# Performance work log

Hardware: AMD Instinct MI355X
Metric: run time of the kernel (lower is better)

Reference implementation:

```python
import jax, jax.numpy as jnp
import numpy as np

B, S, DM, H = 4, 1024, 1024, 16
D = DM // H  # attn_head_size = 64


def setup_inputs() -> dict:
    key = jax.random.key(0)
    ks = jax.random.split(key, 16)
    sc = 0.02
    return {
        "hidden_states": jax.random.normal(ks[0], (B, S, DM), jnp.float32),
        "wq": jax.random.normal(ks[1], (DM, DM), jnp.float32) * sc,
        "bq": jax.random.normal(ks[2], (DM,), jnp.float32) * sc,
        "wk": jax.random.normal(ks[3], (DM, DM), jnp.float32) * sc,
        "bk": jax.random.normal(ks[4], (DM,), jnp.float32) * sc,
        "wv": jax.random.normal(ks[5], (DM, DM), jnp.float32) * sc,
        "bv": jax.random.normal(ks[6], (DM,), jnp.float32) * sc,
        "wo": jax.random.normal(ks[7], (DM, DM), jnp.float32) * sc,
        "bo": jax.random.normal(ks[8], (DM,), jnp.float32) * sc,
        "wfq": jax.random.normal(ks[9], (DM, DM), jnp.float32) * sc,
        "bfq": jax.random.normal(ks[10], (DM,), jnp.float32) * sc,
        "wfg": jax.random.normal(ks[11], (DM, DM), jnp.float32) * sc,
        "bfg": jax.random.normal(ks[12], (DM,), jnp.float32) * sc,
        "up": jax.random.normal(ks[13], (H, 1, D), jnp.float32) * sc,
        "uz": jax.random.normal(ks[14], (H, 1, D), jnp.float32) * sc,
    }


def _split_heads(x):
    # [B, S, DM] -> [B, H, S, D]
    return x.reshape(x.shape[0], x.shape[1], H, D).transpose(0, 2, 1, 3)


def reference(hidden_states, wq, bq, wk, bk, wv, bv, wo, bo,
              wfq, bfq, wfg, bfg, up, uz):
    key_len = hidden_states.shape[1]
    mixed_q = hidden_states @ wq + bq  # [B, S, DM]
    mixed_k = hidden_states @ wk + bk
    mixed_v = hidden_states @ wv + bv

    # focus-attention Gaussian bias
    glo = jnp.mean(mixed_q, axis=1, keepdims=True)                      # [B, 1, DM]
    c = jnp.tanh((mixed_q @ wfq + bfq) + (glo @ wfg + bfg))             # [B, S, DM]
    c = _split_heads(c)                                                 # [B, H, S, D]
    p = jnp.sum(c * up[None], axis=-1)                                  # [B, H, S]
    z = jnp.sum(c * uz[None], axis=-1)                                  # [B, H, S]
    P = jax.nn.sigmoid(p) * key_len                                     # [B, H, S]
    Z = jax.nn.sigmoid(z) * key_len
    j = jnp.arange(key_len, dtype=P.dtype)                              # [S]
    # G[b,h,q,k] = -(k - P[b,h,q])^2 * 2 / Z[b,h,q]^2
    G = -((j[None, None, None, :] - P[..., None]) ** 2) * 2.0 / (Z[..., None] ** 2)

    q = _split_heads(mixed_q)
    k = _split_heads(mixed_k)
    v = _split_heads(mixed_v)

    scores = jnp.einsum("bhqd,bhkd->bhqk", q, k) / jnp.sqrt(jnp.float32(D))
    scores = scores + G
    probs = jax.nn.softmax(scores, axis=-1)  # dropout_prob = 0 -> no-op
    ctx = jnp.einsum("bhqk,bhkd->bhqd", probs, v)
    ctx = ctx.transpose(0, 2, 1, 3).reshape(ctx.shape[0], key_len, H * D)
    return ctx @ wo + bo
```

## Files before the change

kernel.cpp:

```cpp
#include <hip/hip_runtime.h>
#include <hip/hip_bf16.h>
#include <stdint.h>

#define DEV __device__ __forceinline__

typedef __attribute__((ext_vector_type(4))) float f32x4;
typedef __attribute__((ext_vector_type(8))) __bf16 bf16x8;
typedef __attribute__((ext_vector_type(4))) __bf16 bf16x4;
typedef __attribute__((ext_vector_type(4))) unsigned int uint4v;
typedef __attribute__((ext_vector_type(4))) int i32x4;

static constexpr int Bc = 4, Sc = 1024, DMc = 1024, Hc = 16, Dh = 64;
static constexpr int Mc = Bc * Sc;

DEV __bf16 f2b(float x) {
    unsigned u = __builtin_bit_cast(unsigned, x);
    unsigned r = (u + 0x7fffu + ((u >> 16) & 1u)) >> 16;
    return __builtin_bit_cast(__bf16, (unsigned short)r);
}
DEV float b2f(__bf16 x) {
    unsigned short s = __builtin_bit_cast(unsigned short, x);
    unsigned u = ((unsigned)s) << 16;
    return __builtin_bit_cast(float, u);
}
DEV unsigned cvt_pk_bf16(float a, float b) {
    unsigned r;
    asm("v_cvt_pk_bf16_f32 %0, %1, %2" : "=v"(r) : "v"(a), "v"(b));
    return r;
}
DEV void gload_lds16(const void* g, void* l) {
    __builtin_amdgcn_global_load_lds(
        (const __attribute__((address_space(1))) unsigned int*)g,
        (__attribute__((address_space(3))) unsigned int*)l,
        16, 0, 0);
}
DEV bf16x8 ldswz32(const __bf16* base, int row, int lg) {
    const char* p = (const char*)base + row * 64 + (((lg) ^ ((row >> 1) & 3)) << 4);
    return *(const bf16x8*)p;
}

__global__ void k_cvt2(const float* __restrict__ hs, __bf16* __restrict__ hsb,
                       float* __restrict__ part0) {
    int sc = blockIdx.x, b = blockIdx.y, tid = threadIdx.x;
    int c0 = tid * 4;
    float4 s = {0.f, 0.f, 0.f, 0.f};
#pragma unroll
    for (int r = 0; r < 8; r++) {
        size_t row = (size_t)b * 1024 + sc * 8 + r;
        float4 v = *(const float4*)&hs[row * 1024 + c0];
        s.x += v.x; s.y += v.y; s.z += v.z; s.w += v.w;
        bf16x4 o = { f2b(v.x), f2b(v.y), f2b(v.z), f2b(v.w) };
        *(bf16x4*)&hsb[row * 1024 + c0] = o;
    }
    *(float4*)&part0[(size_t)(sc * 4 + b) * 1024 + c0] = s;
}

__global__ void k_tcvt5(const float* __restrict__ s0, const float* __restrict__ s1,
                        const float* __restrict__ s2, const float* __restrict__ s3,
                        const float* __restrict__ s4,
                        __bf16* __restrict__ d0, __bf16* __restrict__ d1,
                        __bf16* __restrict__ d2, __bf16* __restrict__ d3,
                        __bf16* __restrict__ d4, __bf16* __restrict__ wqb) {
    __shared__ float t[32][33];
    const float* in; __bf16* out;
    switch (blockIdx.z) {
        case 0: in = s0; out = d0; break;
        case 1: in = s1; out = d1; break;
        case 2: in = s2; out = d2; break;
        case 3: in = s3; out = d3; break;
        default: in = s4; out = d4; break;
    }
    int c0 = blockIdx.x * 32, r0 = blockIdx.y * 32;
    for (int j = 0; j < 4; j++) {
        float v = in[(size_t)(r0 + threadIdx.y + j * 8) * 1024 + c0 + threadIdx.x];
        t[threadIdx.y + j * 8][threadIdx.x] = v;
        if (blockIdx.z == 0)
            wqb[(size_t)(r0 + threadIdx.y + j * 8) * 1024 + c0 + threadIdx.x] = f2b(v);
    }
    __syncthreads();
    for (int j = 0; j < 4; j++)
        out[(size_t)(c0 + threadIdx.y + j * 8) * 1024 + r0 + threadIdx.x] = f2b(t[threadIdx.x][threadIdx.y + j * 8]);
}

template <int EPI, int BM>
__global__ __launch_bounds__(256) void k_gemm(
    const __bf16* __restrict__ A, const __bf16* __restrict__ Bt,
    const float* __restrict__ bias, void* __restrict__ Cout, int N, int K)
{
    constexpr int MF = BM / 32;
    constexpr int ACH = BM / 64;
    __shared__ __bf16 Al[2][BM * 32];
    __shared__ __bf16 Bl[2][128 * 32];
    const int bm = blockIdx.x, bn = blockIdx.y;
    const int tid = threadIdx.x, lane = tid & 63, wid = tid >> 6;
    const int l15 = lane & 15, lg = lane >> 4;
    const int qr = (wid >> 1) * (BM / 2), qc = (wid & 1) * 64;
    f32x4 acc[MF][4] = {};

    const __bf16* Ab = A + (size_t)bm * BM * K;
    const __bf16* Bb = Bt + (size_t)bn * 128 * K;

#define STAGE_G(k0, dst)                                                          \
    _Pragma("unroll")                                                             \
    for (int c = 0; c < ACH; c++) {                                               \
        int ch = c * 256 + tid, row = ch >> 2, u = ch & 3;                        \
        int su = u ^ ((row >> 1) & 3);                                            \
        gload_lds16(&Ab[(size_t)row * K + (k0) + su * 8], &Al[dst][ch * 8]);      \
    }                                                                             \
    _Pragma("unroll")                                                             \
    for (int c = 0; c < 2; c++) {                                                 \
        int ch = c * 256 + tid, row = ch >> 2, u = ch & 3;                        \
        int su = u ^ ((row >> 1) & 3);                                            \
        gload_lds16(&Bb[(size_t)row * K + (k0) + su * 8], &Bl[dst][ch * 8]);      \
    }

    STAGE_G(0, 0);
    asm volatile("s_waitcnt vmcnt(0)" ::: "memory");
    __builtin_amdgcn_s_barrier();

    int buf = 0;
    for (int t = 0; t < K / 32; t++) {
        if (t + 1 < K / 32) { STAGE_G((t + 1) * 32, buf ^ 1); }
        bf16x8 af[MF], bfv[4];
#pragma unroll
        for (int m = 0; m < MF; m++) af[m] = ldswz32(&Al[buf][0], qr + m * 16 + l15, lg);
#pragma unroll
        for (int n = 0; n < 4; n++) bfv[n] = ldswz32(&Bl[buf][0], qc + n * 16 + l15, lg);
#pragma unroll
        for (int m = 0; m < MF; m++)
#pragma unroll
            for (int n = 0; n < 4; n++)
                acc[m][n] = __builtin_amdgcn_mfma_f32_16x16x32_bf16(af[m], bfv[n], acc[m][n], 0, 0, 0);
        asm volatile("s_waitcnt vmcnt(0)" ::: "memory");
        __builtin_amdgcn_s_barrier();
        buf ^= 1;
    }
#undef STAGE_G
#pragma unroll
    for (int m = 0; m < MF; m++) {
        int row_base = bm * BM + qr + m * 16 + lg * 4;
#pragma unroll
        for (int n = 0; n < 4; n++) {
            int col = bn * 128 + qc + n * 16 + l15;
            float bsum = bias ? bias[col] : 0.0f;
#pragma unroll
            for (int r = 0; r < 4; r++) {
                int row = row_base + r;
                float v = acc[m][n][r] + bsum;
                if constexpr (EPI == 2) ((float*)Cout)[(size_t)row * N + col] = v;
                else ((__bf16*)Cout)[(size_t)row * N + col] = f2b(v);
            }
        }
    }
}

__global__ __launch_bounds__(256) void k_qkvc(
    const __bf16* __restrict__ A, const __bf16* __restrict__ BtAll,
    const float* __restrict__ bq, const float* __restrict__ bk, const float* __restrict__ bv,
    const float* __restrict__ gt2, const float* __restrict__ up, const float* __restrict__ uz,
    __bf16* __restrict__ mq, __bf16* __restrict__ mk_, __bf16* __restrict__ vt,
    float* __restrict__ Pf, float* __restrict__ Zf)
{
    constexpr int K = 1024;
    __shared__ __bf16 Al[2][128 * 32];
    __shared__ __bf16 Bl[2][128 * 32];
    const int bm = blockIdx.x, bn = blockIdx.y;
    const int tid = threadIdx.x, lane = tid & 63, wid = tid >> 6;
    const int l15 = lane & 15, lg = lane >> 4;
    const int qr = (wid >> 1) * 64, qc = (wid & 1) * 64;
    f32x4 acc[4][4] = {};

    const __bf16* Ab = A + (size_t)bm * 128 * K;
    const __bf16* Bb = BtAll + (size_t)bn * 128 * K;

#define STAGE_Q(k0, dst)                                                          \
    _Pragma("unroll")                                                             \
    for (int c = 0; c < 2; c++) {                                                 \
        int ch = c * 256 + tid, row = ch >> 2, u = ch & 3;                        \
        int su = u ^ ((row >> 1) & 3);                                            \
        gload_lds16(&Ab[(size_t)row * K + (k0) + su * 8], &Al[dst][ch * 8]);      \
        gload_lds16(&Bb[(size_t)row * K + (k0) + su * 8], &Bl[dst][ch * 8]);      \
    }

    STAGE_Q(0, 0);
    asm volatile("s_waitcnt vmcnt(0)" ::: "memory");
    __builtin_amdgcn_s_barrier();

    int buf = 0;
    for (int t = 0; t < 32; t++) {
        if (t < 31) { STAGE_Q((t + 1) * 32, buf ^ 1); }
        bf16x8 af[4], bfv[4];
#pragma unroll
        for (int m = 0; m < 4; m++) af[m] = ldswz32(&Al[buf][0], qr + m * 16 + l15, lg);
#pragma unroll
        for (int n = 0; n < 4; n++) bfv[n] = ldswz32(&Bl[buf][0], qc + n * 16 + l15, lg);
#pragma unroll
        for (int m = 0; m < 4; m++)
#pragma unroll
            for (int n = 0; n < 4; n++)
                acc[m][n] = __builtin_amdgcn_mfma_f32_16x16x32_bf16(af[m], bfv[n], acc[m][n], 0, 0, 0);
        asm volatile("s_waitcnt vmcnt(0)" ::: "memory");
        __builtin_amdgcn_s_barrier();
        buf ^= 1;
    }
#undef STAGE_Q

    const int chunk = bn >> 3;
    if (chunk == 3) {
        const int h = (bn & 7) * 2 + (qc >> 6);
        float upv[4], uzv[4];
#pragma unroll
        for (int n = 0; n < 4; n++) {
            upv[n] = up[h * 64 + n * 16 + l15];
            uzv[n] = uz[h * 64 + n * 16 + l15];
        }
#pragma unroll
        for (int m = 0; m < 4; m++) {
            int row_base = bm * 128 + qr + m * 16 + lg * 4;
#pragma unroll
            for (int r = 0; r < 4; r++) {
                int row = row_base + r;
                float p = 0.f, z = 0.f;
#pragma unroll
                for (int n = 0; n < 4; n++) {
                    int col = (bn & 7) * 128 + qc + n * 16 + l15;
                    float cv = tanhf(acc[m][n][r] + gt2[(row >> 10) * 1024 + col]);
                    p += cv * upv[n];
                    z += cv * uzv[n];
                }
#pragma unroll
                for (int d = 1; d < 16; d <<= 1) {
                    p += __shfl_xor(p, d, 16);
                    z += __shfl_xor(z, d, 16);
                }
                if (l15 == 0) {
                    int bb = row >> 10, s = row & 1023;
                    Pf[((size_t)(bb * 16 + h)) * 1024 + s] = 1024.f / (1.f + __expf(-p));
                    Zf[((size_t)(bb * 16 + h)) * 1024 + s] = 1024.f / (1.f + __expf(-z));
                }
            }
        }
    } else if (chunk == 2) {
        const int b = bm >> 3;
#pragma unroll
        for (int m = 0; m < 4; m++) {
            int s0 = (bm & 7) * 128 + qr + m * 16 + lg * 4;
#pragma unroll
            for (int n = 0; n < 4; n++) {
                int col = (bn & 7) * 128 + qc + n * 16 + l15;
                int h = col >> 6, d = col & 63;
                float bsum = bv[col];
                bf16x4 o = { f2b(acc[m][n][0] + bsum), f2b(acc[m][n][1] + bsum),
                             f2b(acc[m][n][2] + bsum), f2b(acc[m][n][3] + bsum) };
                *(bf16x4*)&vt[((size_t)((b * 16 + h) * 64 + d)) * 1024 + s0] = o;
            }
        }
    } else {
        const float* bias = chunk == 0 ? bq : bk;
        __bf16* outp = chunk == 0 ? mq : mk_;
#pragma unroll
        for (int m = 0; m < 4; m++) {
            int row_base = bm * 128 + qr + m * 16 + lg * 4;
#pragma unroll
            for (int n = 0; n < 4; n++) {
                int col = (bn & 7) * 128 + qc + n * 16 + l15;
                float bsum = bias[col];
#pragma unroll
                for (int r = 0; r < 4; r++) {
                    int row = row_base + r;
                    outp[(size_t)row * 1024 + col] = f2b(acc[m][n][r] + bsum);
                }
            }
        }
    }
}

__global__ void k_glo2(const float* __restrict__ part0, const float* __restrict__ wq,
                       float* __restrict__ glo_part) {
    __shared__ float ghs_l[256];
    int tid = threadIdx.x, kc = blockIdx.y;
    {
        int bb = tid >> 6, kk = tid & 63, k = kc * 64 + kk;
        float s = 0.f;
        for (int sc = 0; sc < 128; sc++) s += part0[(size_t)(sc * 4 + bb) * 1024 + k];
        ghs_l[tid] = s * (1.0f / 1024.f);
    }
    __syncthreads();
    int n = blockIdx.x * 256 + tid;
    float a0 = 0, a1 = 0, a2 = 0, a3 = 0;
    for (int j = 0; j < 64; j++) {
        float w = wq[(size_t)(kc * 64 + j) * 1024 + n];
        a0 += ghs_l[j] * w; a1 += ghs_l[64 + j] * w; a2 += ghs_l[128 + j] * w; a3 += ghs_l[192 + j] * w;
    }
    glo_part[(kc * 4 + 0) * 1024 + n] = a0;
    glo_part[(kc * 4 + 1) * 1024 + n] = a1;
    glo_part[(kc * 4 + 2) * 1024 + n] = a2;
    glo_part[(kc * 4 + 3) * 1024 + n] = a3;
}
__global__ void k_gt2p(const float* __restrict__ glo_part, const float* __restrict__ bq,
                       const float* __restrict__ wfg, const float* __restrict__ wfq,
                       float* __restrict__ gt_part) {
    __shared__ float glo_l[256];
    int tid = threadIdx.x, kc = blockIdx.y;
    {
        int bb = tid >> 6, kk = tid & 63, k = kc * 64 + kk;
        float s = bq[k];
        for (int k2 = 0; k2 < 16; k2++) s += glo_part[(k2 * 4 + bb) * 1024 + k];
        glo_l[tid] = s;
    }
    __syncthreads();
    int n = blockIdx.x * 256 + tid;
    float a0 = 0, a1 = 0, a2 = 0, a3 = 0, t = 0;
    for (int j = 0; j < 64; j++) {
        int k = kc * 64 + j;
        float wg = wfg[(size_t)k * 1024 + n];
        float wf = wfq[(size_t)k * 1024 + n];
        a0 += glo_l[j] * wg; a1 += glo_l[64 + j] * wg; a2 += glo_l[128 + j] * wg; a3 += glo_l[192 + j] * wg;
        t += bq[k] * wf;
    }
    gt_part[(kc * 4 + 0) * 1024 + n] = a0 + t;
    gt_part[(kc * 4 + 1) * 1024 + n] = a1 + t;
    gt_part[(kc * 4 + 2) * 1024 + n] = a2 + t;
    gt_part[(kc * 4 + 3) * 1024 + n] = a3 + t;
}
__global__ void k_red_gt(const float* __restrict__ gt_part, const float* __restrict__ bfg,
                         const float* __restrict__ bfq, float* __restrict__ gt2) {
    int i = blockIdx.x * 256 + threadIdx.x;
    int b = i >> 10, n = i & 1023;
    float s = bfg[n] + bfq[n];
    for (int kc = 0; kc < 16; kc++) s += gt_part[(kc * 4 + b) * 1024 + n];
    gt2[i] = s;
}

DEV bf16x8 ldfrag(const __bf16* base, int row, int colbyte) {
    const char* p = (const char*)base + (size_t)row * 128 + (colbyte ^ ((row & 7) << 4));
    return *(const bf16x8*)p;
}

__global__ __launch_bounds__(256) void k_attn(
    const __bf16* __restrict__ Q, const __bf16* __restrict__ Kx, const __bf16* __restrict__ Vt_g,
    const float* __restrict__ Pf, const float* __restrict__ Zf, __bf16* __restrict__ ctx)
{
    __shared__ __bf16 Kl[2][64 * 64];
    __shared__ __bf16 Vl[2][64 * 64];
    const int qt = blockIdx.x, h = blockIdx.y, b = blockIdx.z;
    const int tid = threadIdx.x, lane = tid & 63, wid = tid >> 6;
    const int l15 = lane & 15, lg = lane >> 4;
    const int qbase = qt * 128 + wid * 32;
    const size_t qoff = ((size_t)(b * Sc)) * DMc + h * Dh;

    bf16x8 qf[2][2];
#pragma unroll
    for (int qh = 0; qh < 2; qh++)
#pragma unroll
        for (int dh = 0; dh < 2; dh++)
            qf[qh][dh] = *(const bf16x8*)&Q[qoff + (size_t)(qbase + qh * 16 + l15) * DMc + dh * 32 + lg * 8];

    float Pr[2], Ar[2];
#pragma unroll
    for (int qh = 0; qh < 2; qh++) {
        int row = qbase + qh * 16 + l15;
        float pp = Pf[((size_t)(b * 16 + h)) * 1024 + row];
        float zz = Zf[((size_t)(b * 16 + h)) * 1024 + row];
        Pr[qh] = pp; Ar[qh] = 2.0f / (zz * zz);
    }
    float m[2] = {-1e30f, -1e30f}, l[2] = {0.f, 0.f};
    f32x4 oacc[2][4] = {};

    const __bf16* Kbase = Kx + qoff;
    const __bf16* Vbase = Vt_g + ((size_t)((b * 16 + h) * 64)) * 1024;

#pragma unroll
    for (int i = 0; i < 2; i++) {
        int ch = i * 256 + tid, row = ch >> 3, off = ch & 7;
        uint4v kv = *(const uint4v*)&Kbase[(size_t)row * DMc + off * 8];
        uint4v vv = *(const uint4v*)&Vbase[(size_t)row * 1024 + off * 8];
        *(uint4v*)((char*)&Kl[0][0] + row * 128 + ((off * 16) ^ ((row & 7) << 4))) = kv;
        *(uint4v*)((char*)&Vl[0][0] + row * 128 + ((off * 16) ^ ((row & 7) << 4))) = vv;
    }
    __syncthreads();

    for (int t = 0; t < 16; t++) {
        const int buf = t & 1;
        uint4v rk[2], rv[2];
        if (t < 15) {
#pragma unroll
            for (int i = 0; i < 2; i++) {
                int ch = i * 256 + tid, row = ch >> 3, off = ch & 7;
                rk[i] = *(const uint4v*)&Kbase[(size_t)((t + 1) * 64 + row) * DMc + off * 8];
                rv[i] = *(const uint4v*)&Vbase[(size_t)row * 1024 + (t + 1) * 64 + off * 8];
            }
        }

        f32x4 st[2][4];
        __builtin_amdgcn_s_setprio(1);
#pragma unroll
        for (int c = 0; c < 4; c++) {
            bf16x8 kb0 = ldfrag(&Kl[buf][0], c * 16 + l15, lg * 16);
            bf16x8 kb1 = ldfrag(&Kl[buf][0], c * 16 + l15, 64 + lg * 16);
#pragma unroll
            for (int qh = 0; qh < 2; qh++) {
                f32x4 a = {0.f, 0.f, 0.f, 0.f};
                a = __builtin_amdgcn_mfma_f32_16x16x32_bf16(kb0, qf[qh][0], a, 0, 0, 0);
                a = __builtin_amdgcn_mfma_f32_16x16x32_bf16(kb1, qf[qh][1], a, 0, 0, 0);
                st[qh][c] = a;
            }
        }
        __builtin_amdgcn_s_setprio(0);

        int pk[2][4][2];
#pragma unroll
        for (int qh = 0; qh < 2; qh++) {
            float s[16];
            float mx = -1e30f;
#pragma unroll
            for (int c = 0; c < 4; c++)
#pragma unroll
                for (int r = 0; r < 4; r++) {
                    float kidx = (float)(t * 64 + c * 16 + lg * 4 + r);
                    float dk = kidx - Pr[qh];
                    float v = st[qh][c][r] * 0.125f - dk * dk * Ar[qh];
                    s[c * 4 + r] = v;
                    mx = fmaxf(mx, v);
                }
            mx = fmaxf(mx, __shfl_xor(mx, 16, 64));
            mx = fmaxf(mx, __shfl_xor(mx, 32, 64));
            float nm = fmaxf(m[qh], mx);
            float sc_ = __expf(m[qh] - nm);
            m[qh] = nm;
            float rs = 0.f;
#pragma unroll
            for (int i = 0; i < 16; i++) { float p = __expf(s[i] - nm); s[i] = p; rs += p; }
            rs += __shfl_xor(rs, 16, 64);
            rs += __shfl_xor(rs, 32, 64);
            l[qh] = l[qh] * sc_ + rs;
#pragma unroll
            for (int c = 0; c < 4; c++) {
                pk[qh][c][0] = (int)cvt_pk_bf16(s[c * 4 + 0], s[c * 4 + 1]);
                pk[qh][c][1] = (int)cvt_pk_bf16(s[c * 4 + 2], s[c * 4 + 3]);
            }
#pragma unroll
            for (int r = 0; r < 4; r++) {
                float scr = __shfl(sc_, lg * 4 + r, 16);
#pragma unroll
                for (int dt = 0; dt < 4; dt++) oacc[qh][dt][r] *= scr;
            }
        }

        const int a0 = (((lg & 1) << 1) * 16 + l15) * 4;
        const int a1 = a0 + 64;
        const int selhi = lg >> 1;
#pragma unroll
        for (int kh = 0; kh < 2; kh++) {
            bf16x8 vb[4];
#pragma unroll
            for (int dt = 0; dt < 4; dt++) vb[dt] = ldfrag(&Vl[buf][0], dt * 16 + l15, kh * 64 + lg * 16);
#pragma unroll
            for (int qh = 0; qh < 2; qh++) {
                int w[4];
#pragma unroll
                for (int wi = 0; wi < 4; wi++) {
                    int addr = (wi < 2) ? a0 : a1;
                    int pr = wi & 1;
                    int va = __builtin_amdgcn_ds_bpermute(addr, pk[qh][kh * 2 + 0][pr]);
                    int vb2 = __builtin_amdgcn_ds_bpermute(addr, pk[qh][kh * 2 + 1][pr]);
                    w[wi] = selhi ? vb2 : va;
                }
                i32x4 wv = {w[0], w[1], w[2], w[3]};
                bf16x8 pa = __builtin_bit_cast(bf16x8, wv);
                __builtin_amdgcn_s_setprio(1);
#pragma unroll
                for (int dt = 0; dt < 4; dt++)
                    oacc[qh][dt] = __builtin_amdgcn_mfma_f32_16x16x32_bf16(pa, vb[dt], oacc[qh][dt], 0, 0, 0);
                __builtin_amdgcn_s_setprio(0);
            }
        }

        if (t < 15) {
#pragma unroll
            for (int i = 0; i < 2; i++) {
                int ch = i * 256 + tid, row = ch >> 3, off = ch & 7;
                *(uint4v*)((char*)&Kl[buf ^ 1][0] + row * 128 + ((off * 16) ^ ((row & 7) << 4))) = rk[i];
                *(uint4v*)((char*)&Vl[buf ^ 1][0] + row * 128 + ((off * 16) ^ ((row & 7) << 4))) = rv[i];
            }
        }
        __syncthreads();
    }

#pragma unroll
    for (int qh = 0; qh < 2; qh++) {
        float lr[4];
#pragma unroll
        for (int r = 0; r < 4; r++) lr[r] = __shfl(l[qh], lg * 4 + r, 16);
#pragma unroll
        for (int dt = 0; dt < 4; dt++)
#pragma unroll
            for (int r = 0; r < 4; r++) {
                int row = qbase + qh * 16 + lg * 4 + r;
                ctx[((size_t)(b * Sc) + row) * DMc + h * Dh + dt * 16 + l15] =
                    f2b(oacc[qh][dt][r] / lr[r]);
            }
    }
}

extern "C" void kernel_launch(void* const* d_in, const int* in_sizes, int n_in,
                              void* d_out, int out_size, void* d_ws, size_t ws_size,
                              hipStream_t stream) {
    const float* hs  = (const float*)d_in[0];
    const float* wq  = (const float*)d_in[1];
    const float* bq  = (const float*)d_in[2];
    const float* wk  = (const float*)d_in[3];
    const float* bk  = (const float*)d_in[4];
    const float* wv  = (const float*)d_in[5];
    const float* bv  = (const float*)d_in[6];
    const float* wo  = (const float*)d_in[7];
    const float* bo  = (const float*)d_in[8];
    const float* wfq = (const float*)d_in[9];
    const float* bfq = (const float*)d_in[10];
    const float* wfg = (const float*)d_in[11];
    const float* bfg = (const float*)d_in[12];
    const float* up  = (const float*)d_in[13];
    const float* uz  = (const float*)d_in[14];

    char* ws = (char*)d_ws;
    const size_t MB = 1ull << 20;
    __bf16* hsb   = (__bf16*)(ws);
    __bf16* BtAll = (__bf16*)(ws + 8 * MB);
    __bf16* wfqT  = (__bf16*)(ws + 16 * MB);
    __bf16* woT   = (__bf16*)(ws + 18 * MB);
    __bf16* mq    = (__bf16*)(ws + 20 * MB);
    __bf16* mk    = (__bf16*)(ws + 28 * MB);
    __bf16* vt    = (__bf16*)(ws + 36 * MB);
    __bf16* ctxb  = (__bf16*)(ws);
    __bf16* wqb   = (__bf16*)(ws + 55 * MB);
    char* sm = ws + 52 * MB;
    float* Pf       = (float*)(sm);
    float* Zf       = (float*)(sm + (256 << 10));
    float* glo_part = (float*)(sm + (512 << 10));
    float* gt_part  = (float*)(sm + (768 << 10));
    float* gt2      = (float*)(sm + (1024 << 10));
    float* part0    = (float*)(ws + 57 * MB);

    k_cvt2<<<dim3(128, 4), 256, 0, stream>>>(hs, hsb, part0);
    k_tcvt5<<<dim3(32, 32, 5), dim3(32, 8), 0, stream>>>(
        wq, wk, wv, wfq, wo,
        BtAll, BtAll + 1048576, BtAll + 2097152, wfqT, woT, wqb);

    k_glo2<<<dim3(4, 16), 256, 0, stream>>>(part0, wq, glo_part);
    k_gt2p<<<dim3(4, 16), 256, 0, stream>>>(glo_part, bq, wfg, wfq, gt_part);
    k_red_gt<<<16, 256, 0, stream>>>(gt_part, bfg, bfq, gt2);

    k_gemm<0, 64><<<dim3(16, 8), 256, 0, stream>>>(wfqT, wqb, nullptr, BtAll + 3145728, DMc, DMc);

    k_qkvc<<<dim3(32, 32), 256, 0, stream>>>(hsb, BtAll, bq, bk, bv, gt2, up, uz,
                                             mq, mk, vt, Pf, Zf);

    k_attn<<<dim3(8, 16, 4), 256, 0, stream>>>(mq, mk, vt, Pf, Zf, ctxb);

    k_gemm<2, 64><<<dim3(64, 8), 256, 0, stream>>>(ctxb, woT, bo, d_out, DMc, DMc);
}
```

Baseline: 193.1 us.

## Triple-buffer LDS staging in projection GEMMs with prefetch distance two

Both the generic GEMM and the fused QKV/focus GEMM move from double to triple LDS buffers and issue global-to-LDS loads two K-steps ahead. Each step now waits only until the current tile's loads have landed, using a partial vmcnt count, so the next tile's loads stay in flight through the MFMA work. This hides more global load latency behind compute. The cost is 50% more LDS per block, which can lower occupancy, and per-block-size wait counts that only exist for the block sizes already specialised.

```diff
diff --git a/kernel.cpp b/kernel.cpp
--- a/kernel.cpp
+++ b/kernel.cpp
@@ -34,6 +34,11 @@
         (__attribute__((address_space(3))) unsigned int*)l,
         16, 0, 0);
 }
+template <int N> DEV void wvm();
+template <> DEV void wvm<0>() { asm volatile("s_waitcnt vmcnt(0)" ::: "memory"); }
+template <> DEV void wvm<3>() { asm volatile("s_waitcnt vmcnt(3)" ::: "memory"); }
+template <> DEV void wvm<4>() { asm volatile("s_waitcnt vmcnt(4)" ::: "memory"); }
+
 DEV bf16x8 ldswz32(const __bf16* base, int row, int lg) {
     const char* p = (const char*)base + row * 64 + (((lg) ^ ((row >> 1) & 3)) << 4);
     return *(const bf16x8*)p;
@@ -89,8 +94,8 @@
 {
     constexpr int MF = BM / 32;
     constexpr int ACH = BM / 64;
-    __shared__ __bf16 Al[2][BM * 32];
-    __shared__ __bf16 Bl[2][128 * 32];
+    __shared__ __bf16 Al[3][BM * 32];
+    __shared__ __bf16 Bl[3][128 * 32];
     const int bm = blockIdx.x, bn = blockIdx.y;
     const int tid = threadIdx.x, lane = tid & 63, wid = tid >> 6;
     const int l15 = lane & 15, lg = lane >> 4;
@@ -100,40 +105,45 @@
     const __bf16* Ab = A + (size_t)bm * BM * K;
     const __bf16* Bb = Bt + (size_t)bn * 128 * K;
 
-#define STAGE_G(k0, dst)                                                          \
+#define STAGE_G(k0, Ad, Bd)                                                       \
     _Pragma("unroll")                                                             \
     for (int c = 0; c < ACH; c++) {                                               \
         int ch = c * 256 + tid, row = ch >> 2, u = ch & 3;                        \
         int su = u ^ ((row >> 1) & 3);                                            \
-        gload_lds16(&Ab[(size_t)row * K + (k0) + su * 8], &Al[dst][ch * 8]);      \
+        gload_lds16(&Ab[(size_t)row * K + (k0) + su * 8], (Ad) + ch * 8);         \
     }                                                                             \
     _Pragma("unroll")                                                             \
     for (int c = 0; c < 2; c++) {                                                 \
         int ch = c * 256 + tid, row = ch >> 2, u = ch & 3;                        \
         int su = u ^ ((row >> 1) & 3);                                            \
-        gload_lds16(&Bb[(size_t)row * K + (k0) + su * 8], &Bl[dst][ch * 8]);      \
-    }
-
-    STAGE_G(0, 0);
-    asm volatile("s_waitcnt vmcnt(0)" ::: "memory");
+        gload_lds16(&Bb[(size_t)row * K + (k0) + su * 8], (Bd) + ch * 8);         \
+    }
+
+    const int T = K / 32;
+    STAGE_G(0, &Al[0][0], &Bl[0][0]);
+    STAGE_G(32, &Al[1][0], &Bl[1][0]);
+    wvm<ACH + 2>();
     __builtin_amdgcn_s_barrier();
 
-    int buf = 0;
-    for (int t = 0; t < K / 32; t++) {
-        if (t + 1 < K / 32) { STAGE_G((t + 1) * 32, buf ^ 1); }
+    int rd = 0, st = 2;
+    for (int t = 0; t < T; t++) {
+        if (t + 2 < T) { STAGE_G((t + 2) * 32, &Al[st][0], &Bl[st][0]); }
+        const __bf16* Ar = &Al[rd][0];
+        const __bf16* Br = &Bl[rd][0];
         bf16x8 af[MF], bfv[4];
 #pragma unroll
-        for (int m = 0; m < MF; m++) af[m] = ldswz32(&Al[buf][0], qr + m * 16 + l15, lg);
-#pragma unroll
-        for (int n = 0; n < 4; n++) bfv[n] = ldswz32(&Bl[buf][0], qc + n * 16 + l15, lg);
+        for (int m = 0; m < MF; m++) af[m] = ldswz32(Ar, qr + m * 16 + l15, lg);
+#pragma unroll
+        for (int n = 0; n < 4; n++) bfv[n] = ldswz32(Br, qc + n * 16 + l15, lg);
 #pragma unroll
         for (int m = 0; m < MF; m++)
 #pragma unroll
             for (int n = 0; n < 4; n++)
                 acc[m][n] = __builtin_amdgcn_mfma_f32_16x16x32_bf16(af[m], bfv[n], acc[m][n], 0, 0, 0);
-        asm volatile("s_waitcnt vmcnt(0)" ::: "memory");
+        if (t + 2 < T) wvm<ACH + 2>(); else wvm<0>();
         __builtin_amdgcn_s_barrier();
-        buf ^= 1;
+        rd = rd == 2 ? 0 : rd + 1;
+        st = st == 2 ? 0 : st + 1;
     }
 #undef STAGE_G
 #pragma unroll
@@ -162,8 +172,8 @@
     float* __restrict__ Pf, float* __restrict__ Zf)
 {
     constexpr int K = 1024;
-    __shared__ __bf16 Al[2][128 * 32];
-    __shared__ __bf16 Bl[2][128 * 32];
+    __shared__ __bf16 Al[3][128 * 32];
+    __shared__ __bf16 Bl[3][128 * 32];
     const int bm = blockIdx.x, bn = blockIdx.y;
     const int tid = threadIdx.x, lane = tid & 63, wid = tid >> 6;
     const int l15 = lane & 15, lg = lane >> 4;
@@ -173,35 +183,39 @@
     const __bf16* Ab = A + (size_t)bm * 128 * K;
     const __bf16* Bb = BtAll + (size_t)bn * 128 * K;
 
-#define STAGE_Q(k0, dst)                                                          \
+#define STAGE_Q(k0, Ad, Bd)                                                       \
     _Pragma("unroll")                                                             \
     for (int c = 0; c < 2; c++) {                                                 \
         int ch = c * 256 + tid, row = ch >> 2, u = ch & 3;                        \
         int su = u ^ ((row >> 1) & 3);                                            \
-        gload_lds16(&Ab[(size_t)row * K + (k0) + su * 8], &Al[dst][ch * 8]);      \
-        gload_lds16(&Bb[(size_t)row * K + (k0) + su * 8], &Bl[dst][ch * 8]);      \
-    }
-
-    STAGE_Q(0, 0);
-    asm volatile("s_waitcnt vmcnt(0)" ::: "memory");
+        gload_lds16(&Ab[(size_t)row * K + (k0) + su * 8], (Ad) + ch * 8);         \
+        gload_lds16(&Bb[(size_t)row * K + (k0) + su * 8], (Bd) + ch * 8);         \
+    }
+
+    STAGE_Q(0, &Al[0][0], &Bl[0][0]);
+    STAGE_Q(32, &Al[1][0], &Bl[1][0]);
+    wvm<4>();
     __builtin_amdgcn_s_barrier();
 
-    int buf = 0;
+    int rd = 0, st = 2;
     for (int t = 0; t < 32; t++) {
-        if (t < 31) { STAGE_Q((t + 1) * 32, buf ^ 1); }
+        if (t + 2 < 32) { STAGE_Q((t + 2) * 32, &Al[st][0], &Bl[st][0]); }
+        const __bf16* Ar = &Al[rd][0];
+        const __bf16* Br = &Bl[rd][0];
         bf16x8 af[4], bfv[4];
 #pragma unroll
-        for (int m = 0; m < 4; m++) af[m] = ldswz32(&Al[buf][0], qr + m * 16 + l15, lg);
-#pragma unroll
-        for (int n = 0; n < 4; n++) bfv[n] = ldswz32(&Bl[buf][0], qc + n * 16 + l15, lg);
+        for (int m = 0; m < 4; m++) af[m] = ldswz32(Ar, qr + m * 16 + l15, lg);
+#pragma unroll
+        for (int n = 0; n < 4; n++) bfv[n] = ldswz32(Br, qc + n * 16 + l15, lg);
 #pragma unroll
         for (int m = 0; m < 4; m++)
 #pragma unroll
             for (int n = 0; n < 4; n++)
                 acc[m][n] = __builtin_amdgcn_mfma_f32_16x16x32_bf16(af[m], bfv[n], acc[m][n], 0, 0, 0);
-        asm volatile("s_waitcnt vmcnt(0)" ::: "memory");
+        if (t + 2 < 32) wvm<4>(); else wvm<0>();
         __builtin_amdgcn_s_barrier();
-        buf ^= 1;
+        rd = rd == 2 ? 0 : rd + 1;
+        st = st == 2 ? 0 : st + 1;
     }
 #undef STAGE_Q
 
```

Result: no change. 189.7 us (-1.8%).
